# Performance work log

Hardware: AMD Instinct MI355X
Metric: run time of the kernel (lower is better)

The kernel has to match this reference:

```python
import jax, jax.numpy as jnp
import numpy as np

N_NODES = 100_000
N_EDGES = 1_600_000
IN_C, HID_C, OUT_C = 128, 64, 32


def gcn_conv(x, W, b, src, dst, n_nodes):
    """PyG GCNConv with add_self_loops=True, symmetric normalization.
    out = D^{-1/2} (A + I) D^{-1/2} (x @ W) + b, with D = deg(A) + 1.
    Self-loop contribution added analytically to avoid materializing loop edges."""
    h = x @ W                                            # [N, F_out]
    deg = jnp.zeros((n_nodes,), h.dtype).at[dst].add(1.0) + 1.0
    dinv = jax.lax.rsqrt(deg)                            # deg >= 1 from self-loops
    norm = dinv[src] * dinv[dst]                         # [E]
    agg = jnp.zeros_like(h).at[dst].add(h[src] * norm[:, None])
    agg = agg + h * (dinv * dinv)[:, None]               # self-loop term
    return agg + b


def setup_inputs() -> dict:
    key = jax.random.key(0)
    ks = jax.random.split(key, 9)
    x = jax.random.normal(ks[0], (N_NODES, IN_C), dtype=jnp.float32)
    edge_index = jax.random.randint(ks[1], (2, N_EDGES), 0, N_NODES, dtype=jnp.int64)
    g = lambda k, fi, fo: jax.random.normal(k, (fi, fo), jnp.float32) * np.sqrt(2.0 / (fi + fo)).astype(np.float32)
    W1 = g(ks[2], IN_C, HID_C)
    b1 = jnp.zeros((HID_C,), jnp.float32)
    W2 = g(ks[3], HID_C, OUT_C)
    b2 = jnp.zeros((OUT_C,), jnp.float32)
    Wl = g(ks[4], IN_C + HID_C + OUT_C, OUT_C)
    bl = jnp.zeros((OUT_C,), jnp.float32)
    return {"x": x, "edge_index": edge_index, "W1": W1, "b1": b1,
            "W2": W2, "b2": b2, "Wl": Wl, "bl": bl}


def reference(x, edge_index, W1, b1, W2, b2, Wl, bl):
    src, dst = edge_index[0], edge_index[1]
    n = x.shape[0]
    h1 = jax.nn.relu(gcn_conv(x, W1, b1, src, dst, n))   # dropout is identity in eval
    h2 = gcn_conv(h1, W2, b2, src, dst, n)
    cat = jnp.concatenate([x, h1, h2], axis=1)           # [N, in+hid+out]
    return jax.nn.log_softmax(cat @ Wl + bl, axis=-1)
```

## Files before the change

kernel.cpp:

```cpp
#include <hip/hip_runtime.h>
#include <hip/hip_bf16.h>
#include <hip/hip_fp16.h>

typedef __hip_bfloat16 bf16;
typedef __attribute__((ext_vector_type(8))) short short8;
typedef __attribute__((ext_vector_type(4))) float f32x4;

#define MFMA16(a, b, c) __builtin_amdgcn_mfma_f32_16x16x32_bf16((a), (b), (c), 0, 0, 0)

static __device__ __forceinline__ float ldf(const void* p, long long i, bool f32) {
    return f32 ? ((const float*)p)[i] : __bfloat162float(((const bf16*)p)[i]);
}

static __device__ __forceinline__ short f2bs(float v) {
    union { bf16 h; short s; } u; u.h = __float2bfloat16(v); return u.s;
}

static __device__ __forceinline__ unsigned int pack_bf16x2(float a, float b) {
    return (unsigned int)(unsigned short)f2bs(a) | ((unsigned int)(unsigned short)f2bs(b) << 16);
}

__global__ __launch_bounds__(256, 4)
void sniff_kernel(const void* __restrict__ x, const void* __restrict__ w,
                  const int* __restrict__ ei, int E, int* __restrict__ flags) {
    __shared__ int cnt;
    if (threadIdx.x == 0) cnt = 0;
    __syncthreads();
    if (blockIdx.x < 2) {
        const unsigned short* u = (const unsigned short*)(blockIdx.x == 0 ? x : w);
        int bad = 0;
        for (int i = threadIdx.x; i < 4096; i += 256) {
            unsigned e = (u[i] >> 7) & 0xFF;
            if (e >= 0xA0) bad++;
        }
        atomicAdd(&cnt, bad);
        __syncthreads();
        if (threadIdx.x == 0) flags[blockIdx.x] = (cnt > 16) ? 1 : 0;
    } else {
        int nz = 0;
        for (int i = threadIdx.x; i < 1024; i += 256)
            if (ei[2 * i + 1] != 0) nz++;
        atomicAdd(&cnt, nz);
        __syncthreads();
        if (threadIdx.x == 0) flags[2] = (cnt == 0) ? 1 : 0;
    }
}

static __device__ __forceinline__ int ld_src(const int* ei, int E, int e, bool i64) {
    return i64 ? ei[2 * e] : ei[e];
}
static __device__ __forceinline__ int ld_dst(const int* ei, int E, int e, bool i64) {
    return i64 ? ei[2 * (E + e)] : ei[E + e];
}


__global__ __launch_bounds__(256, 4)
void bhist_kernel(const int* __restrict__ ei, int E, const int* __restrict__ flags,
                  int shift, int NB, int* __restrict__ bucketCount) {
    __shared__ int h[256];
    for (int i = threadIdx.x; i < 256; i += 256) h[i] = 0;
    __syncthreads();
    bool i64 = flags[2] != 0;
    int base = blockIdx.x * 4096;
    for (int i = 0; i < 16; i++) {
        int e = base + i * 256 + threadIdx.x;
        if (e < E) atomicAdd(&h[ld_dst(ei, E, e, i64) >> shift], 1);
    }
    __syncthreads();
    for (int i = threadIdx.x; i < NB; i += 256)
        if (h[i]) atomicAdd(&bucketCount[i], h[i]);
}

__global__ __launch_bounds__(256, 4)
void bscan_kernel(const int* __restrict__ bucketCount, int NB,
                  int* __restrict__ bucketBase, int* __restrict__ bcursor, int E) {
    __shared__ int bs[256];
    int v = ((int)threadIdx.x < NB) ? bucketCount[threadIdx.x] : 0;
    bs[threadIdx.x] = v;
    __syncthreads();
    for (int off = 1; off < 256; off <<= 1) {
        int t = ((int)threadIdx.x >= off) ? bs[threadIdx.x - off] : 0;
        __syncthreads();
        bs[threadIdx.x] += t;
        __syncthreads();
    }
    int excl = bs[threadIdx.x] - v;
    if ((int)threadIdx.x < NB) { bucketBase[threadIdx.x] = excl; bcursor[threadIdx.x] = excl; }
    if (threadIdx.x == 0) bucketBase[NB] = E;
}

__global__ __launch_bounds__(256, 4)
void bpart_kernel(const int* __restrict__ ei, int E, const int* __restrict__ flags,
                  int shift, int NB, int* __restrict__ bcursor, int2* __restrict__ ebuf) {
    __shared__ int h[256];
    __shared__ int gofs[256];
    __shared__ int2 se[4096];
    for (int i = threadIdx.x; i < 256; i += 256) h[i] = 0;
    __syncthreads();
    bool i64 = flags[2] != 0;
    int base = blockIdx.x * 4096;
    for (int i = 0; i < 16; i++) {
        int e = base + i * 256 + threadIdx.x;
        if (e < E) {
            int s = ld_src(ei, E, e, i64), d = ld_dst(ei, E, e, i64);
            se[i * 256 + threadIdx.x] = make_int2(s, d);
            atomicAdd(&h[d >> shift], 1);
        }
    }
    __syncthreads();
    if ((int)threadIdx.x < NB) {
        int c = h[threadIdx.x];
        gofs[threadIdx.x] = c ? atomicAdd(&bcursor[threadIdx.x], c) : 0;
    }
    __syncthreads();
    for (int i = threadIdx.x; i < 256; i += 256) h[i] = 0;
    __syncthreads();
    for (int i = 0; i < 16; i++) {
        int e = base + i * 256 + threadIdx.x;
        if (e < E) {
            int2 v = se[i * 256 + threadIdx.x];
            int b = v.y >> shift;
            int p = atomicAdd(&h[b], 1);
            ebuf[gofs[b] + p] = v;
        }
    }
}

__global__ __launch_bounds__(256, 2)
void bbuild_kernel(const int2* __restrict__ ebuf, const int* __restrict__ bucketBase,
                   int shift, int N, int E, int* __restrict__ rowptr,
                   float* __restrict__ dinv, int* __restrict__ csr_src) {
    __shared__ int cnt[1024];
    __shared__ int exc[1024];
    __shared__ int bs[256];
    int b = blockIdx.x;
    int nodeBase = b << shift;
    int width = 1 << shift;
    int nn = N - nodeBase; if (nn > width) nn = width;
    int beg = bucketBase[b], end = bucketBase[b + 1];
    for (int i = threadIdx.x; i < width; i += 256) cnt[i] = 0;
    __syncthreads();
    for (int e = beg + threadIdx.x; e < end; e += 256)
        atomicAdd(&cnt[ebuf[e].y - nodeBase], 1);
    __syncthreads();
    int per = width / 256;
    int s = 0;
    int base4 = threadIdx.x * per;
    for (int i = 0; i < per; i++) s += cnt[base4 + i];
    bs[threadIdx.x] = s;
    __syncthreads();
    for (int off = 1; off < 256; off <<= 1) {
        int t = ((int)threadIdx.x >= off) ? bs[threadIdx.x - off] : 0;
        __syncthreads();
        bs[threadIdx.x] += t;
        __syncthreads();
    }
    int run = bs[threadIdx.x] - s;
    for (int i = 0; i < per; i++) { exc[base4 + i] = run; run += cnt[base4 + i]; }
    __syncthreads();
    for (int i = threadIdx.x; i < nn; i += 256) {
        int node = nodeBase + i;
        rowptr[node] = beg + exc[i];
        dinv[node] = rsqrtf((float)cnt[i] + 1.0f);
    }
    __syncthreads();
    for (int i = threadIdx.x; i < width; i += 256) cnt[i] = 0;
    __syncthreads();
    for (int e = beg + threadIdx.x; e < end; e += 256) {
        int2 v = ebuf[e];
        int l = v.y - nodeBase;
        int p = atomicAdd(&cnt[l], 1);
        csr_src[beg + exc[l] + p] = v.x;
    }
    if (b == 0 && threadIdx.x == 0) rowptr[N] = E;
}

__global__ __launch_bounds__(256, 4)
void repack_kernel(const void* __restrict__ W1, const void* __restrict__ W2,
                   const void* __restrict__ Wl, const int* __restrict__ flags,
                   bf16* __restrict__ Bp1, bf16* __restrict__ Bp2, bf16* __restrict__ Bp3) {
    bool fw = flags[1] != 0;
    const void* W; bf16* Bp; int ntiles, nc, nfrag;
    if (blockIdx.x == 0)      { W = W1; Bp = Bp1; ntiles = 4; nc = 64; nfrag = 16; }
    else if (blockIdx.x == 1) { W = W2; Bp = Bp2; ntiles = 2; nc = 32; nfrag = 4;  }
    else                      { W = Wl; Bp = Bp3; ntiles = 2; nc = 32; nfrag = 14; }
    for (int s = threadIdx.x; s < nfrag * 64; s += 256) {
        int f = s >> 6, lane = s & 63;
        int kstep = f / ntiles, ntile = f % ntiles;
        int n = ntile * 16 + (lane & 15);
        int kbase = kstep * 32 + (lane >> 4) * 8;
#pragma unroll
        for (int j = 0; j < 8; j++)
            Bp[s * 8 + j] = __float2bfloat16(ldf(W, (long long)(kbase + j) * nc + n, fw));
    }
}

__global__ __launch_bounds__(256, 3)
void gemm1_mfma_kernel(const void* __restrict__ x, const bf16* __restrict__ Bpack,
                       const float* __restrict__ dinv, const int* __restrict__ flags,
                       __half* __restrict__ h1g, short* __restrict__ xb, int N) {
    bool fx = flags[0] != 0;
    int lane = threadIdx.x & 63, wave = threadIdx.x >> 6;
    int m = lane & 15, quad = lane >> 4;
    int base = blockIdx.x * 128 + wave * 32;
    if (base >= N) return;
    const short8* bp = (const short8*)Bpack;
    short8 B[16];
#pragma unroll
    for (int i = 0; i < 16; i++) B[i] = bp[i * 64 + lane];
    if (base + 32 <= N) {
#pragma unroll
        for (int t = 0; t < 2; t++) {
            int r0 = base + t * 16;
            short8 A[4];
            if (fx) {
                const float* xr = &((const float*)x)[(long long)(r0 + m) * 128 + quad * 8];
#pragma unroll
                for (int k = 0; k < 4; k++) {
                    float4 fa = *(const float4*)(xr + k * 32);
                    float4 fb = *(const float4*)(xr + k * 32 + 4);
                    short8 o;
                    o[0] = f2bs(fa.x); o[1] = f2bs(fa.y); o[2] = f2bs(fa.z); o[3] = f2bs(fa.w);
                    o[4] = f2bs(fb.x); o[5] = f2bs(fb.y); o[6] = f2bs(fb.z); o[7] = f2bs(fb.w);
                    A[k] = o;
                }
                short* xw = &xb[(long long)(r0 + m) * 128 + quad * 8];
#pragma unroll
                for (int k = 0; k < 4; k++) *(short8*)(xw + k * 32) = A[k];
            } else {
                const short* xr = &((const short*)x)[(long long)(r0 + m) * 128 + quad * 8];
#pragma unroll
                for (int k = 0; k < 4; k++) A[k] = *(const short8*)(xr + k * 32);
            }
            f32x4 acc[4];
#pragma unroll
            for (int nt = 0; nt < 4; nt++) acc[nt] = (f32x4){0.f, 0.f, 0.f, 0.f};
#pragma unroll
            for (int k = 0; k < 4; k++) {
#pragma unroll
                for (int nt = 0; nt < 4; nt++) acc[nt] = MFMA16(A[k], B[k * 4 + nt], acc[nt]);
            }
            float dv[4];
#pragma unroll
            for (int r = 0; r < 4; r++) dv[r] = dinv[r0 + quad * 4 + r];
            __half* o = &h1g[(long long)(r0 + quad * 4) * 64 + m];
#pragma unroll
            for (int nt = 0; nt < 4; nt++) {
#pragma unroll
                for (int r = 0; r < 4; r++) o[(long long)r * 64 + nt * 16] = __float2half(acc[nt][r] * dv[r]);
            }
        }
    } else {
#pragma unroll
        for (int t = 0; t < 2; t++) {
            int r0 = base + t * 16;
            int row = r0 + m;
            short8 A[4];
#pragma unroll
            for (int k = 0; k < 4; k++) A[k] = (short8){0,0,0,0,0,0,0,0};
            if (row < N) {
                if (fx) {
                    const float* xr = &((const float*)x)[(long long)row * 128 + quad * 8];
#pragma unroll
                    for (int k = 0; k < 4; k++) {
                        float4 fa = *(const float4*)(xr + k * 32);
                        float4 fb = *(const float4*)(xr + k * 32 + 4);
                        short8 o;
                        o[0] = f2bs(fa.x); o[1] = f2bs(fa.y); o[2] = f2bs(fa.z); o[3] = f2bs(fa.w);
                        o[4] = f2bs(fb.x); o[5] = f2bs(fb.y); o[6] = f2bs(fb.z); o[7] = f2bs(fb.w);
                        A[k] = o;
                    }
                    short* xw = &xb[(long long)row * 128 + quad * 8];
#pragma unroll
                    for (int k = 0; k < 4; k++) *(short8*)(xw + k * 32) = A[k];
                } else {
                    const short* xr = &((const short*)x)[(long long)row * 128 + quad * 8];
#pragma unroll
                    for (int k = 0; k < 4; k++) A[k] = *(const short8*)(xr + k * 32);
                }
            }
            f32x4 acc[4];
#pragma unroll
            for (int nt = 0; nt < 4; nt++) acc[nt] = (f32x4){0.f, 0.f, 0.f, 0.f};
#pragma unroll
            for (int k = 0; k < 4; k++) {
#pragma unroll
                for (int nt = 0; nt < 4; nt++) acc[nt] = MFMA16(A[k], B[k * 4 + nt], acc[nt]);
            }
#pragma unroll
            for (int r = 0; r < 4; r++) {
                int orow = r0 + quad * 4 + r;
                if (orow < N) {
                    float dv = dinv[orow];
                    __half* o = &h1g[(long long)orow * 64 + m];
#pragma unroll
                    for (int nt = 0; nt < 4; nt++) o[nt * 16] = __float2half(acc[nt][r] * dv);
                }
            }
        }
    }
}

__global__ __launch_bounds__(256, 8)
void gather1_kernel(const unsigned int* __restrict__ h1g, const float* __restrict__ dinv,
                    const int* __restrict__ rowptr, const int* __restrict__ csr_src,
                    const void* __restrict__ bptr, const int* __restrict__ flags,
                    unsigned int* __restrict__ h1b, int N) {
    bool fw = flags[1] != 0;
    int lane = threadIdx.x & 63;
    int c = lane & 31, hf = lane >> 5;
    int wv = __builtin_amdgcn_readfirstlane(threadIdx.x >> 6);
    int n0 = (blockIdx.x * 4 + wv) * 2;
    if (n0 >= N) return;
    bool has1 = (n0 + 1 < N);
    int beg = rowptr[n0];
    int mid = rowptr[n0 + 1];
    int end = has1 ? rowptr[n0 + 2] : mid;
    const unsigned int* hL = h1g + c;
    float aA0 = 0.f, aA1 = 0.f;
    float aN0 = 0.f, aN1 = 0.f;
    int p = beg;
    for (; p + 32 <= end; p += 32) {
        unsigned int v[16]; float r[16];
#pragma unroll
        for (int u = 0; u < 16; u++) {
            int s0 = csr_src[p + 2 * u];
            int s1 = csr_src[p + 2 * u + 1];
            int s = hf ? s1 : s0;
            r[u] = ((p + 2 * u + hf) < mid) ? 1.f : 0.f;
            v[u] = hL[(long long)s * 32];
        }
#pragma unroll
        for (int u = 0; u < 16; u++) {
            float2 f = __half22float2(*(const __half2*)&v[u]);
            aA0 += f.x; aA1 += f.y;
            aN0 = fmaf(f.x, r[u], aN0);
            aN1 = fmaf(f.y, r[u], aN1);
        }
    }
    for (; p + 16 <= end; p += 16) {
        unsigned int v[8]; float r[8];
#pragma unroll
        for (int u = 0; u < 8; u++) {
            int s0 = csr_src[p + 2 * u];
            int s1 = csr_src[p + 2 * u + 1];
            int s = hf ? s1 : s0;
            r[u] = ((p + 2 * u + hf) < mid) ? 1.f : 0.f;
            v[u] = hL[(long long)s * 32];
        }
#pragma unroll
        for (int u = 0; u < 8; u++) {
            float2 f = __half22float2(*(const __half2*)&v[u]);
            aA0 += f.x; aA1 += f.y;
            aN0 = fmaf(f.x, r[u], aN0);
            aN1 = fmaf(f.y, r[u], aN1);
        }
    }
    if (p < end) {
        unsigned int v[8]; float mk[8], r[8];
#pragma unroll
        for (int u = 0; u < 8; u++) {
            int i0 = p + 2 * u, i1 = i0 + 1;
            int s0 = csr_src[(i0 < end) ? i0 : beg];
            int s1 = csr_src[(i1 < end) ? i1 : beg];
            int s = hf ? s1 : s0;
            int i = p + 2 * u + hf;
            mk[u] = (i < end) ? 1.f : 0.f;
            r[u]  = (i < mid) ? 1.f : 0.f;
            v[u] = hL[(long long)s * 32];
        }
#pragma unroll
        for (int u = 0; u < 8; u++) {
            float2 f = __half22float2(*(const __half2*)&v[u]);
            aA0 = fmaf(f.x, mk[u], aA0);
            aA1 = fmaf(f.y, mk[u], aA1);
            aN0 = fmaf(f.x, r[u], aN0);
            aN1 = fmaf(f.y, r[u], aN1);
        }
    }
    aA0 += __shfl_xor(aA0, 32); aA1 += __shfl_xor(aA1, 32);
    aN0 += __shfl_xor(aN0, 32); aN1 += __shfl_xor(aN1, 32);
    int node = n0 + hf;
    if (node < N) {
        float a0 = hf ? (aA0 - aN0) : aN0;
        float a1 = hf ? (aA1 - aN1) : aN1;
        unsigned int gsv = h1g[(long long)node * 32 + c];
        float2 gs = __half22float2(*(const __half2*)&gsv);
        float dvd = dinv[node];
        float o0 = dvd * (a0 + gs.x) + ldf(bptr, 2 * c, fw);
        float o1 = dvd * (a1 + gs.y) + ldf(bptr, 2 * c + 1, fw);
        h1b[(long long)node * 32 + c] = pack_bf16x2(fmaxf(o0, 0.f), fmaxf(o1, 0.f));
    }
}

__global__ __launch_bounds__(256, 4)
void gemm2_mfma_kernel(const short* __restrict__ h1b, const bf16* __restrict__ Bpack,
                       const float* __restrict__ dinv, __half* __restrict__ h2g, int N) {
    int lane = threadIdx.x & 63, wave = threadIdx.x >> 6;
    int m = lane & 15, quad = lane >> 4;
    int r0 = blockIdx.x * 64 + wave * 16;
    if (r0 >= N) return;
    const short8* bp = (const short8*)Bpack;
    short8 B[4];
#pragma unroll
    for (int i = 0; i < 4; i++) B[i] = bp[i * 64 + lane];
    f32x4 acc0 = {0.f,0.f,0.f,0.f}, acc1 = {0.f,0.f,0.f,0.f};
    if (r0 + 16 <= N) {
        const short* xr = &h1b[(long long)(r0 + m) * 64 + quad * 8];
#pragma unroll
        for (int k = 0; k < 2; k++) {
            short8 A = *(const short8*)(xr + k * 32);
            acc0 = MFMA16(A, B[k * 2 + 0], acc0);
            acc1 = MFMA16(A, B[k * 2 + 1], acc1);
        }
        float dv[4];
#pragma unroll
        for (int r = 0; r < 4; r++) dv[r] = dinv[r0 + quad * 4 + r];
        __half* o = &h2g[(long long)(r0 + quad * 4) * 32 + m];
#pragma unroll
        for (int r = 0; r < 4; r++) {
            o[(long long)r * 32]      = __float2half(acc0[r] * dv[r]);
            o[(long long)r * 32 + 16] = __float2half(acc1[r] * dv[r]);
        }
    } else {
        int row = r0 + m;
#pragma unroll
        for (int k = 0; k < 2; k++) {
            short8 A = {0,0,0,0,0,0,0,0};
            if (row < N) A = *(const short8*)&h1b[(long long)row * 64 + k * 32 + quad * 8];
            acc0 = MFMA16(A, B[k * 2 + 0], acc0);
            acc1 = MFMA16(A, B[k * 2 + 1], acc1);
        }
#pragma unroll
        for (int r = 0; r < 4; r++) {
            int orow = r0 + quad * 4 + r;
            if (orow < N) {
                float dv = dinv[orow];
                h2g[(long long)orow * 32 + m]      = __float2half(acc0[r] * dv);
                h2g[(long long)orow * 32 + 16 + m] = __float2half(acc1[r] * dv);
            }
        }
    }
}

__global__ __launch_bounds__(256, 8)
void gather2_kernel(const unsigned int* __restrict__ h2g, const float* __restrict__ dinv,
                    const int* __restrict__ rowptr, const int* __restrict__ csr_src,
                    const void* __restrict__ bptr, const int* __restrict__ flags,
                    unsigned int* __restrict__ h2b, int N) {
    bool fw = flags[1] != 0;
    int lane = threadIdx.x & 63;
    int c = lane & 15, sub = lane >> 4;
    int wv = __builtin_amdgcn_readfirstlane(threadIdx.x >> 6);
    int n0 = (blockIdx.x * 4 + wv) * 2;
    if (n0 >= N) return;
    bool has1 = (n0 + 1 < N);
    int beg = rowptr[n0];
    int mid = rowptr[n0 + 1];
    int end = has1 ? rowptr[n0 + 2] : mid;
    const unsigned int* hL = h2g + c;
    float aA0 = 0.f, aA1 = 0.f, aN0 = 0.f, aN1 = 0.f;
    int p = beg;
    for (; p + 32 <= end; p += 32) {
        unsigned int v[8]; float r[8];
#pragma unroll
        for (int u = 0; u < 8; u++) {
            int i0 = p + 4 * u;
            int sa0 = csr_src[i0], sa1 = csr_src[i0 + 1];
            int sa2 = csr_src[i0 + 2], sa3 = csr_src[i0 + 3];
            int sA = (sub & 1) ? sa1 : sa0;
            int sB = (sub & 1) ? sa3 : sa2;
            int s  = (sub & 2) ? sB : sA;
            r[u] = ((i0 + sub) < mid) ? 1.f : 0.f;
            v[u] = hL[(long long)s * 16];
        }
#pragma unroll
        for (int u = 0; u < 8; u++) {
            float2 f = __half22float2(*(const __half2*)&v[u]);
            aA0 += f.x; aA1 += f.y;
            aN0 = fmaf(f.x, r[u], aN0);
            aN1 = fmaf(f.y, r[u], aN1);
        }
    }
    for (; p + 16 <= end; p += 16) {
        unsigned int v[4]; float r[4];
#pragma unroll
        for (int u = 0; u < 4; u++) {
            int i0 = p + 4 * u;
            int sa0 = csr_src[i0], sa1 = csr_src[i0 + 1];
            int sa2 = csr_src[i0 + 2], sa3 = csr_src[i0 + 3];
            int sA = (sub & 1) ? sa1 : sa0;
            int sB = (sub & 1) ? sa3 : sa2;
            int s  = (sub & 2) ? sB : sA;
            r[u] = ((i0 + sub) < mid) ? 1.f : 0.f;
            v[u] = hL[(long long)s * 16];
        }
#pragma unroll
        for (int u = 0; u < 4; u++) {
            float2 f = __half22float2(*(const __half2*)&v[u]);
            aA0 += f.x; aA1 += f.y;
            aN0 = fmaf(f.x, r[u], aN0);
            aN1 = fmaf(f.y, r[u], aN1);
        }
    }
    if (p < end) {
        unsigned int v[4]; float mk[4], r[4];
#pragma unroll
        for (int u = 0; u < 4; u++) {
            int i0 = p + 4 * u;
            int sa0 = csr_src[(i0     < end) ? i0     : beg];
            int sa1 = csr_src[(i0 + 1 < end) ? i0 + 1 : beg];
            int sa2 = csr_src[(i0 + 2 < end) ? i0 + 2 : beg];
            int sa3 = csr_src[(i0 + 3 < end) ? i0 + 3 : beg];
            int sA = (sub & 1) ? sa1 : sa0;
            int sB = (sub & 1) ? sa3 : sa2;
            int s  = (sub & 2) ? sB : sA;
            int i = i0 + sub;
            mk[u] = (i < end) ? 1.f : 0.f;
            r[u]  = (i < mid) ? 1.f : 0.f;
            v[u] = hL[(long long)s * 16];
        }
#pragma unroll
        for (int u = 0; u < 4; u++) {
            float2 f = __half22float2(*(const __half2*)&v[u]);
            aA0 = fmaf(f.x, mk[u], aA0);
            aA1 = fmaf(f.y, mk[u], aA1);
            aN0 = fmaf(f.x, r[u], aN0);
            aN1 = fmaf(f.y, r[u], aN1);
        }
    }
    aA0 += __shfl_xor(aA0, 16); aA1 += __shfl_xor(aA1, 16);
    aN0 += __shfl_xor(aN0, 16); aN1 += __shfl_xor(aN1, 16);
    aA0 += __shfl_xor(aA0, 32); aA1 += __shfl_xor(aA1, 32);
    aN0 += __shfl_xor(aN0, 32); aN1 += __shfl_xor(aN1, 32);
    if (sub < 2) {
        int node = n0 + sub;
        if (node < N) {
            float a0 = sub ? (aA0 - aN0) : aN0;
            float a1 = sub ? (aA1 - aN1) : aN1;
            unsigned int gsv = h2g[(long long)node * 16 + c];
            float2 gs = __half22float2(*(const __half2*)&gsv);
            float dvd = dinv[node];
            float o0 = dvd * (a0 + gs.x) + ldf(bptr, 2 * c, fw);
            float o1 = dvd * (a1 + gs.y) + ldf(bptr, 2 * c + 1, fw);
            h2b[(long long)node * 16 + c] = pack_bf16x2(o0, o1);
        }
    }
}

__global__ __launch_bounds__(256, 2)
void final_mfma_kernel(const void* __restrict__ x, const short* __restrict__ xb,
                       const short* __restrict__ h1b,
                       const short* __restrict__ h2b, const bf16* __restrict__ Bpack,
                       const void* __restrict__ bl, const int* __restrict__ flags,
                       void* __restrict__ out, int N) {
    bool fw = flags[1] != 0, fx = flags[0] != 0;
    const short* xs = fx ? xb : (const short*)x;
    int lane = threadIdx.x & 63, wave = threadIdx.x >> 6;
    int m = lane & 15, quad = lane >> 4;
    int r0 = blockIdx.x * 64 + wave * 16;
    if (r0 >= N) return;
    const short8* bp = (const short8*)Bpack;
    short8 B[14];
#pragma unroll
    for (int i = 0; i < 14; i++) B[i] = bp[i * 64 + lane];
    f32x4 acc0 = {0.f,0.f,0.f,0.f}, acc1 = {0.f,0.f,0.f,0.f};
    bool full = (r0 + 16 <= N);
    int row = r0 + m;
    bool rowok = full || (row < N);
#pragma unroll
    for (int s = 0; s < 7; s++) {
        short8 A = {0,0,0,0,0,0,0,0};
        if (rowok) {
            const short* p;
            if (s < 4)      p = &xs [(long long)row * 128 + s * 32 + quad * 8];
            else if (s < 6) p = &h1b[(long long)row * 64 + (s - 4) * 32 + quad * 8];
            else            p = &h2b[(long long)row * 32 + quad * 8];
            A = *(const short8*)p;
        }
        acc0 = MFMA16(A, B[s * 2 + 0], acc0);
        acc1 = MFMA16(A, B[s * 2 + 1], acc1);
    }
    float bl0 = ldf(bl, m, fw), bl1 = ldf(bl, m + 16, fw);
#pragma unroll
    for (int r = 0; r < 4; r++) {
        float v0 = acc0[r] + bl0, v1 = acc1[r] + bl1;
        float mx = fmaxf(v0, v1);
#pragma unroll
        for (int o = 8; o > 0; o >>= 1) mx = fmaxf(mx, __shfl_xor(mx, o));
        float sm = __expf(v0 - mx) + __expf(v1 - mx);
#pragma unroll
        for (int o = 8; o > 0; o >>= 1) sm += __shfl_xor(sm, o);
        float lse = mx + __logf(sm);
        int orow = r0 + quad * 4 + r;
        if (orow < N) {
            if (fx) {
                ((float*)out)[(long long)orow * 32 + m]      = v0 - lse;
                ((float*)out)[(long long)orow * 32 + 16 + m] = v1 - lse;
            } else {
                ((bf16*)out)[(long long)orow * 32 + m]      = __float2bfloat16(v0 - lse);
                ((bf16*)out)[(long long)orow * 32 + 16 + m] = __float2bfloat16(v1 - lse);
            }
        }
    }
}

extern "C" void kernel_launch(void* const* d_in, const int* in_sizes, int n_in,
                              void* d_out, int out_size, void* d_ws, size_t ws_size,
                              hipStream_t stream) {
    const void* x  = d_in[0];
    const int*  ei = (const int*)d_in[1];
    const void* W1 = d_in[2];
    const void* b1 = d_in[3];
    const void* W2 = d_in[4];
    const void* b2 = d_in[5];
    const void* Wl = d_in[6];
    const void* bl = d_in[7];

    int N = in_sizes[0] / 128;
    int E = in_sizes[1] / 2;

    int shift = 9;
    while (((N + (1 << shift) - 1) >> shift) > 256 && shift < 10) shift++;
    int NB = (N + (1 << shift) - 1) >> shift;

    int* ip      = (int*)d_ws;
    int* flags   = ip;
    int* bucketCount = ip + 16;
    int* bucketBase  = bucketCount + 256;
    int* bcursor     = bucketBase + 272;
    float* dinv  = (float*)(bcursor + 256);
    int* rowptr  = (int*)(dinv + N);
    bf16* Bp1    = (bf16*)(rowptr + N + 16);
    bf16* Bp2    = (bf16*)((int*)Bp1 + 4096);
    bf16* Bp3    = (bf16*)((int*)Bp2 + 1024);
    int* csr_src = (int*)Bp3 + 3584;
    short* xb    = (short*)(csr_src + E);
    int*   Ai    = (int*)xb + (size_t)N * 64;
    int2*  ebuf  = (int2*)Ai;
    __half* h1g  = (__half*)Ai;
    __half* h2g  = (__half*)Ai;
    unsigned int* h2b = (unsigned int*)(Ai + (size_t)N * 48);
    unsigned int* h1b = (unsigned int*)(Ai + (size_t)N * 64);

    hipMemsetAsync(ip, 0, (16 + 256) * sizeof(int), stream);

    sniff_kernel<<<3, 256, 0, stream>>>(x, W1, ei, E, flags);

    int nchunk = (E + 4095) / 4096;
    bhist_kernel<<<nchunk, 256, 0, stream>>>(ei, E, flags, shift, NB, bucketCount);
    bscan_kernel<<<1, 256, 0, stream>>>(bucketCount, NB, bucketBase, bcursor, E);
    bpart_kernel<<<nchunk, 256, 0, stream>>>(ei, E, flags, shift, NB, bcursor, ebuf);
    bbuild_kernel<<<NB, 256, 0, stream>>>(ebuf, bucketBase, shift, N, E, rowptr, dinv, csr_src);

    repack_kernel<<<3, 256, 0, stream>>>(W1, W2, Wl, flags, Bp1, Bp2, Bp3);

    gemm1_mfma_kernel<<<(N + 127) / 128, 256, 0, stream>>>(x, Bp1, dinv, flags, h1g, xb, N);
    gather1_kernel<<<(N + 7) / 8, 256, 0, stream>>>((const unsigned int*)h1g, dinv, rowptr, csr_src,
                                                    b1, flags, h1b, N);
    gemm2_mfma_kernel<<<(N + 63) / 64, 256, 0, stream>>>((const short*)h1b, Bp2, dinv, h2g, N);
    gather2_kernel<<<(N + 7) / 8, 256, 0, stream>>>((const unsigned int*)h2g, dinv, rowptr, csr_src,
                                                    b2, flags, h2b, N);
    final_mfma_kernel<<<(N + 63) / 64, 256, 0, stream>>>(x, (const short*)xb, (const short*)h1b,
                                                         (const short*)h2b, Bp3, bl, flags, d_out, N);
}
```

Baseline: 293.2 us.

## Fuse sniff/repack/scan kernels and fold second-layer GEMM into gather1

Merges the dtype sniff and weight repack into the bucket-histogram launch, and drops the separate bucket-scan kernel. Each partition and build block now recomputes the prefix sum itself, and each block re-detects the index width. The layer-2 GEMM is computed inside gather1 as an FP32 dot product against W2 staged in shared memory, which removes the gemm2 launch and a round trip of h1 through global memory. The cost is redundant per-block scans and W2 loads, more LDS use in gather1 that may lower occupancy, and scalar FMA instead of MFMA for the 64x32 product.

```diff
diff --git a/kernel.cpp b/kernel.cpp
--- a/kernel.cpp
+++ b/kernel.cpp
@@ -20,48 +20,78 @@
     return (unsigned int)(unsigned short)f2bs(a) | ((unsigned int)(unsigned short)f2bs(b) << 16);
 }
 
+static __device__ __forceinline__ int ld_src(const int* ei, int E, int e, bool i64) {
+    return i64 ? ei[2 * e] : ei[e];
+}
+static __device__ __forceinline__ int ld_dst(const int* ei, int E, int e, bool i64) {
+    return i64 ? ei[2 * (E + e)] : ei[E + e];
+}
+
+
 __global__ __launch_bounds__(256, 4)
-void sniff_kernel(const void* __restrict__ x, const void* __restrict__ w,
-                  const int* __restrict__ ei, int E, int* __restrict__ flags) {
-    __shared__ int cnt;
-    if (threadIdx.x == 0) cnt = 0;
-    __syncthreads();
-    if (blockIdx.x < 2) {
-        const unsigned short* u = (const unsigned short*)(blockIdx.x == 0 ? x : w);
+void bhist_kernel(const int* __restrict__ ei, int E,
+                  const void* __restrict__ x, const void* __restrict__ W1,
+                  const void* __restrict__ Wl,
+                  int shift, int NB, int nchunk,
+                  int* __restrict__ flags, int* __restrict__ bucketCount,
+                  bf16* __restrict__ Bp1, bf16* __restrict__ Bp3) {
+    __shared__ int h[256];
+    __shared__ int sdet;
+    int bid = blockIdx.x;
+    if (bid >= nchunk) {
+        int which = bid - nchunk;
+        const void* W = which ? Wl : W1;
+        bf16* Bp = which ? Bp3 : Bp1;
+        int ntiles = which ? 2 : 4, nc = which ? 32 : 64, nfrag = which ? 14 : 16;
+        if (threadIdx.x == 0) sdet = 0;
+        __syncthreads();
+        const unsigned short* u = (const unsigned short*)W;
         int bad = 0;
         for (int i = threadIdx.x; i < 4096; i += 256) {
             unsigned e = (u[i] >> 7) & 0xFF;
             if (e >= 0xA0) bad++;
         }
-        atomicAdd(&cnt, bad);
-        __syncthreads();
-        if (threadIdx.x == 0) flags[blockIdx.x] = (cnt > 16) ? 1 : 0;
-    } else {
+        if (bad) atomicAdd(&sdet, bad);
+        __syncthreads();
+        bool fw = sdet > 16;
+        if (which == 0 && threadIdx.x == 0) flags[1] = fw ? 1 : 0;
+        for (int s = threadIdx.x; s < nfrag * 64; s += 256) {
+            int f = s >> 6, lane = s & 63;
+            int kstep = f / ntiles, ntile = f % ntiles;
+            int n = ntile * 16 + (lane & 15);
+            int kbase = kstep * 32 + (lane >> 4) * 8;
+#pragma unroll
+            for (int j = 0; j < 8; j++)
+                Bp[s * 8 + j] = __float2bfloat16(ldf(W, (long long)(kbase + j) * nc + n, fw));
+        }
+        return;
+    }
+    if (bid == 0) {
+        if (threadIdx.x == 0) sdet = 0;
+        __syncthreads();
+        const unsigned short* u = (const unsigned short*)x;
+        int bad = 0;
+        for (int i = threadIdx.x; i < 4096; i += 256) {
+            unsigned e = (u[i] >> 7) & 0xFF;
+            if (e >= 0xA0) bad++;
+        }
+        if (bad) atomicAdd(&sdet, bad);
+        __syncthreads();
+        if (threadIdx.x == 0) flags[0] = (sdet > 16) ? 1 : 0;
+        __syncthreads();
+    }
+    if (threadIdx.x == 0) sdet = 0;
+    for (int i = threadIdx.x; i < 256; i += 256) h[i] = 0;
+    __syncthreads();
+    {
         int nz = 0;
         for (int i = threadIdx.x; i < 1024; i += 256)
-            if (ei[2 * i + 1] != 0) nz++;
-        atomicAdd(&cnt, nz);
-        __syncthreads();
-        if (threadIdx.x == 0) flags[2] = (cnt == 0) ? 1 : 0;
-    }
-}
-
-static __device__ __forceinline__ int ld_src(const int* ei, int E, int e, bool i64) {
-    return i64 ? ei[2 * e] : ei[e];
-}
-static __device__ __forceinline__ int ld_dst(const int* ei, int E, int e, bool i64) {
-    return i64 ? ei[2 * (E + e)] : ei[E + e];
-}
-
-
-__global__ __launch_bounds__(256, 4)
-void bhist_kernel(const int* __restrict__ ei, int E, const int* __restrict__ flags,
-                  int shift, int NB, int* __restrict__ bucketCount) {
-    __shared__ int h[256];
-    for (int i = threadIdx.x; i < 256; i += 256) h[i] = 0;
-    __syncthreads();
-    bool i64 = flags[2] != 0;
-    int base = blockIdx.x * 4096;
+            if (2 * i + 1 < 2 * E && ei[2 * i + 1] != 0) nz++;
+        if (nz) atomicAdd(&sdet, nz);
+    }
+    __syncthreads();
+    bool i64 = (sdet == 0);
+    int base = bid * 4096;
     for (int i = 0; i < 16; i++) {
         int e = base + i * 256 + threadIdx.x;
         if (e < E) atomicAdd(&h[ld_dst(ei, E, e, i64) >> shift], 1);
@@ -72,32 +102,25 @@
 }
 
 __global__ __launch_bounds__(256, 4)
-void bscan_kernel(const int* __restrict__ bucketCount, int NB,
-                  int* __restrict__ bucketBase, int* __restrict__ bcursor, int E) {
-    __shared__ int bs[256];
-    int v = ((int)threadIdx.x < NB) ? bucketCount[threadIdx.x] : 0;
-    bs[threadIdx.x] = v;
-    __syncthreads();
-    for (int off = 1; off < 256; off <<= 1) {
-        int t = ((int)threadIdx.x >= off) ? bs[threadIdx.x - off] : 0;
-        __syncthreads();
-        bs[threadIdx.x] += t;
-        __syncthreads();
-    }
-    int excl = bs[threadIdx.x] - v;
-    if ((int)threadIdx.x < NB) { bucketBase[threadIdx.x] = excl; bcursor[threadIdx.x] = excl; }
-    if (threadIdx.x == 0) bucketBase[NB] = E;
-}
-
-__global__ __launch_bounds__(256, 4)
-void bpart_kernel(const int* __restrict__ ei, int E, const int* __restrict__ flags,
-                  int shift, int NB, int* __restrict__ bcursor, int2* __restrict__ ebuf) {
+void bpart_kernel(const int* __restrict__ ei, int E, int shift, int NB,
+                  const int* __restrict__ bucketCount, int* __restrict__ bcursor,
+                  int2* __restrict__ ebuf) {
     __shared__ int h[256];
     __shared__ int gofs[256];
+    __shared__ int bs[256];
     __shared__ int2 se[4096];
+    __shared__ int sdet;
+    if (threadIdx.x == 0) sdet = 0;
     for (int i = threadIdx.x; i < 256; i += 256) h[i] = 0;
     __syncthreads();
-    bool i64 = flags[2] != 0;
+    {
+        int nz = 0;
+        for (int i = threadIdx.x; i < 1024; i += 256)
+            if (2 * i + 1 < 2 * E && ei[2 * i + 1] != 0) nz++;
+        if (nz) atomicAdd(&sdet, nz);
+    }
+    __syncthreads();
+    bool i64 = (sdet == 0);
     int base = blockIdx.x * 4096;
     for (int i = 0; i < 16; i++) {
         int e = base + i * 256 + threadIdx.x;
@@ -107,10 +130,19 @@
             atomicAdd(&h[d >> shift], 1);
         }
     }
-    __syncthreads();
+    int v = ((int)threadIdx.x < NB) ? bucketCount[threadIdx.x] : 0;
+    bs[threadIdx.x] = v;
+    __syncthreads();
+    for (int off = 1; off < 256; off <<= 1) {
+        int t = ((int)threadIdx.x >= off) ? bs[threadIdx.x - off] : 0;
+        __syncthreads();
+        bs[threadIdx.x] += t;
+        __syncthreads();
+    }
     if ((int)threadIdx.x < NB) {
         int c = h[threadIdx.x];
-        gofs[threadIdx.x] = c ? atomicAdd(&bcursor[threadIdx.x], c) : 0;
+        int b0 = bs[threadIdx.x] - v;
+        gofs[threadIdx.x] = c ? (b0 + atomicAdd(&bcursor[threadIdx.x], c)) : 0;
     }
     __syncthreads();
     for (int i = threadIdx.x; i < 256; i += 256) h[i] = 0;
@@ -118,26 +150,37 @@
     for (int i = 0; i < 16; i++) {
         int e = base + i * 256 + threadIdx.x;
         if (e < E) {
-            int2 v = se[i * 256 + threadIdx.x];
-            int b = v.y >> shift;
+            int2 w = se[i * 256 + threadIdx.x];
+            int b = w.y >> shift;
             int p = atomicAdd(&h[b], 1);
-            ebuf[gofs[b] + p] = v;
+            ebuf[gofs[b] + p] = w;
         }
     }
 }
 
 __global__ __launch_bounds__(256, 2)
-void bbuild_kernel(const int2* __restrict__ ebuf, const int* __restrict__ bucketBase,
+void bbuild_kernel(const int2* __restrict__ ebuf, const int* __restrict__ bucketCount,
                    int shift, int N, int E, int* __restrict__ rowptr,
                    float* __restrict__ dinv, int* __restrict__ csr_src) {
     __shared__ int cnt[1024];
     __shared__ int exc[1024];
     __shared__ int bs[256];
     int b = blockIdx.x;
+    int v = ((int)threadIdx.x < 256) ? bucketCount[threadIdx.x] : 0;
+    bs[threadIdx.x] = v;
+    __syncthreads();
+    for (int off = 1; off < 256; off <<= 1) {
+        int t = ((int)threadIdx.x >= off) ? bs[threadIdx.x - off] : 0;
+        __syncthreads();
+        bs[threadIdx.x] += t;
+        __syncthreads();
+    }
+    int end = bs[b];
+    int beg = end - bucketCount[b];
+    __syncthreads();
     int nodeBase = b << shift;
     int width = 1 << shift;
     int nn = N - nodeBase; if (nn > width) nn = width;
-    int beg = bucketBase[b], end = bucketBase[b + 1];
     for (int i = threadIdx.x; i < width; i += 256) cnt[i] = 0;
     __syncthreads();
     for (int e = beg + threadIdx.x; e < end; e += 256)
@@ -167,32 +210,12 @@
     for (int i = threadIdx.x; i < width; i += 256) cnt[i] = 0;
     __syncthreads();
     for (int e = beg + threadIdx.x; e < end; e += 256) {
-        int2 v = ebuf[e];
-        int l = v.y - nodeBase;
+        int2 w = ebuf[e];
+        int l = w.y - nodeBase;
         int p = atomicAdd(&cnt[l], 1);
-        csr_src[beg + exc[l] + p] = v.x;
+        csr_src[beg + exc[l] + p] = w.x;
     }
     if (b == 0 && threadIdx.x == 0) rowptr[N] = E;
-}
-
-__global__ __launch_bounds__(256, 4)
-void repack_kernel(const void* __restrict__ W1, const void* __restrict__ W2,
-                   const void* __restrict__ Wl, const int* __restrict__ flags,
-                   bf16* __restrict__ Bp1, bf16* __restrict__ Bp2, bf16* __restrict__ Bp3) {
-    bool fw = flags[1] != 0;
-    const void* W; bf16* Bp; int ntiles, nc, nfrag;
-    if (blockIdx.x == 0)      { W = W1; Bp = Bp1; ntiles = 4; nc = 64; nfrag = 16; }
-    else if (blockIdx.x == 1) { W = W2; Bp = Bp2; ntiles = 2; nc = 32; nfrag = 4;  }
-    else                      { W = Wl; Bp = Bp3; ntiles = 2; nc = 32; nfrag = 14; }
-    for (int s = threadIdx.x; s < nfrag * 64; s += 256) {
-        int f = s >> 6, lane = s & 63;
-        int kstep = f / ntiles, ntile = f % ntiles;
-        int n = ntile * 16 + (lane & 15);
-        int kbase = kstep * 32 + (lane >> 4) * 8;
-#pragma unroll
-        for (int j = 0; j < 8; j++)
-            Bp[s * 8 + j] = __float2bfloat16(ldf(W, (long long)(kbase + j) * nc + n, fw));
-    }
 }
 
 __global__ __launch_bounds__(256, 3)
@@ -304,9 +327,15 @@
 __global__ __launch_bounds__(256, 8)
 void gather1_kernel(const unsigned int* __restrict__ h1g, const float* __restrict__ dinv,
                     const int* __restrict__ rowptr, const int* __restrict__ csr_src,
-                    const void* __restrict__ bptr, const int* __restrict__ flags,
-                    unsigned int* __restrict__ h1b, int N) {
+                    const void* __restrict__ bptr, const void* __restrict__ W2,
+                    const int* __restrict__ flags,
+                    unsigned int* __restrict__ h1b, __half* __restrict__ h2g, int N) {
+    __shared__ float w2s[64 * 32];
+    __shared__ float h1s[4][2][64];
     bool fw = flags[1] != 0;
+    for (int i = threadIdx.x; i < 2048; i += 256)
+        w2s[i] = ldf(W2, i, fw);
+    __syncthreads();
     int lane = threadIdx.x & 63;
     int c = lane & 31, hf = lane >> 5;
     int wv = __builtin_amdgcn_readfirstlane(threadIdx.x >> 6);
@@ -381,66 +410,26 @@
     aA0 += __shfl_xor(aA0, 32); aA1 += __shfl_xor(aA1, 32);
     aN0 += __shfl_xor(aN0, 32); aN1 += __shfl_xor(aN1, 32);
     int node = n0 + hf;
-    if (node < N) {
-        float a0 = hf ? (aA0 - aN0) : aN0;
-        float a1 = hf ? (aA1 - aN1) : aN1;
-        unsigned int gsv = h1g[(long long)node * 32 + c];
-        float2 gs = __half22float2(*(const __half2*)&gsv);
-        float dvd = dinv[node];
-        float o0 = dvd * (a0 + gs.x) + ldf(bptr, 2 * c, fw);
-        float o1 = dvd * (a1 + gs.y) + ldf(bptr, 2 * c + 1, fw);
-        h1b[(long long)node * 32 + c] = pack_bf16x2(fmaxf(o0, 0.f), fmaxf(o1, 0.f));
-    }
-}
-
-__global__ __launch_bounds__(256, 4)
-void gemm2_mfma_kernel(const short* __restrict__ h1b, const bf16* __restrict__ Bpack,
-                       const float* __restrict__ dinv, __half* __restrict__ h2g, int N) {
-    int lane = threadIdx.x & 63, wave = threadIdx.x >> 6;
-    int m = lane & 15, quad = lane >> 4;
-    int r0 = blockIdx.x * 64 + wave * 16;
-    if (r0 >= N) return;
-    const short8* bp = (const short8*)Bpack;
-    short8 B[4];
-#pragma unroll
-    for (int i = 0; i < 4; i++) B[i] = bp[i * 64 + lane];
-    f32x4 acc0 = {0.f,0.f,0.f,0.f}, acc1 = {0.f,0.f,0.f,0.f};
-    if (r0 + 16 <= N) {
-        const short* xr = &h1b[(long long)(r0 + m) * 64 + quad * 8];
-#pragma unroll
-        for (int k = 0; k < 2; k++) {
-            short8 A = *(const short8*)(xr + k * 32);
-            acc0 = MFMA16(A, B[k * 2 + 0], acc0);
-            acc1 = MFMA16(A, B[k * 2 + 1], acc1);
-        }
-        float dv[4];
-#pragma unroll
-        for (int r = 0; r < 4; r++) dv[r] = dinv[r0 + quad * 4 + r];
-        __half* o = &h2g[(long long)(r0 + quad * 4) * 32 + m];
-#pragma unroll
-        for (int r = 0; r < 4; r++) {
-            o[(long long)r * 32]      = __float2half(acc0[r] * dv[r]);
-            o[(long long)r * 32 + 16] = __float2half(acc1[r] * dv[r]);
-        }
-    } else {
-        int row = r0 + m;
-#pragma unroll
-        for (int k = 0; k < 2; k++) {
-            short8 A = {0,0,0,0,0,0,0,0};
-            if (row < N) A = *(const short8*)&h1b[(long long)row * 64 + k * 32 + quad * 8];
-            acc0 = MFMA16(A, B[k * 2 + 0], acc0);
-            acc1 = MFMA16(A, B[k * 2 + 1], acc1);
-        }
-#pragma unroll
-        for (int r = 0; r < 4; r++) {
-            int orow = r0 + quad * 4 + r;
-            if (orow < N) {
-                float dv = dinv[orow];
-                h2g[(long long)orow * 32 + m]      = __float2half(acc0[r] * dv);
-                h2g[(long long)orow * 32 + 16 + m] = __float2half(acc1[r] * dv);
-            }
-        }
-    }
+    int nodeC = (node < N) ? node : n0;
+    float a0 = hf ? (aA0 - aN0) : aN0;
+    float a1 = hf ? (aA1 - aN1) : aN1;
+    unsigned int gsv = h1g[(long long)nodeC * 32 + c];
+    float2 gs = __half22float2(*(const __half2*)&gsv);
+    float dvd = dinv[nodeC];
+    float o0 = fmaxf(dvd * (a0 + gs.x) + ldf(bptr, 2 * c, fw), 0.f);
+    float o1 = fmaxf(dvd * (a1 + gs.y) + ldf(bptr, 2 * c + 1, fw), 0.f);
+    if (node < N)
+        h1b[(long long)node * 32 + c] = pack_bf16x2(o0, o1);
+    h1s[wv][hf][2 * c]     = o0;
+    h1s[wv][hf][2 * c + 1] = o1;
+    __threadfence_block();
+    const float* hrow = h1s[wv][hf];
+    float acc = 0.f;
+#pragma unroll 8
+    for (int k = 0; k < 64; k++)
+        acc = fmaf(hrow[k], w2s[k * 32 + c], acc);
+    if (node < N)
+        h2g[(long long)node * 32 + c] = __float2half(dvd * acc);
 }
 
 __global__ __launch_bounds__(256, 8)
@@ -639,26 +628,21 @@
     int*   Ai    = (int*)xb + (size_t)N * 64;
     int2*  ebuf  = (int2*)Ai;
     __half* h1g  = (__half*)Ai;
-    __half* h2g  = (__half*)Ai;
+    __half* h2g  = (__half*)(Ai + (size_t)N * 32);
     unsigned int* h2b = (unsigned int*)(Ai + (size_t)N * 48);
     unsigned int* h1b = (unsigned int*)(Ai + (size_t)N * 64);
 
-    hipMemsetAsync(ip, 0, (16 + 256) * sizeof(int), stream);
-
-    sniff_kernel<<<3, 256, 0, stream>>>(x, W1, ei, E, flags);
+    hipMemsetAsync(ip, 0, 800 * sizeof(int), stream);
 
     int nchunk = (E + 4095) / 4096;
-    bhist_kernel<<<nchunk, 256, 0, stream>>>(ei, E, flags, shift, NB, bucketCount);
-    bscan_kernel<<<1, 256, 0, stream>>>(bucketCount, NB, bucketBase, bcursor, E);
-    bpart_kernel<<<nchunk, 256, 0, stream>>>(ei, E, flags, shift, NB, bcursor, ebuf);
-    bbuild_kernel<<<NB, 256, 0, stream>>>(ebuf, bucketBase, shift, N, E, rowptr, dinv, csr_src);
-
-    repack_kernel<<<3, 256, 0, stream>>>(W1, W2, Wl, flags, Bp1, Bp2, Bp3);
+    bhist_kernel<<<nchunk + 2, 256, 0, stream>>>(ei, E, x, W1, Wl, shift, NB, nchunk,
+                                                 flags, bucketCount, Bp1, Bp3);
+    bpart_kernel<<<nchunk, 256, 0, stream>>>(ei, E, shift, NB, bucketCount, bcursor, ebuf);
+    bbuild_kernel<<<NB, 256, 0, stream>>>(ebuf, bucketCount, shift, N, E, rowptr, dinv, csr_src);
 
     gemm1_mfma_kernel<<<(N + 127) / 128, 256, 0, stream>>>(x, Bp1, dinv, flags, h1g, xb, N);
     gather1_kernel<<<(N + 7) / 8, 256, 0, stream>>>((const unsigned int*)h1g, dinv, rowptr, csr_src,
-                                                    b1, flags, h1b, N);
-    gemm2_mfma_kernel<<<(N + 63) / 64, 256, 0, stream>>>((const short*)h1b, Bp2, dinv, h2g, N);
+                                                    b1, W2, flags, h1b, h2g, N);
     gather2_kernel<<<(N + 7) / 8, 256, 0, stream>>>((const unsigned int*)h2g, dinv, rowptr, csr_src,
                                                     b2, flags, h2b, N);
     final_mfma_kernel<<<(N + 63) / 64, 256, 0, stream>>>(x, (const short*)xb, (const short*)h1b,
```

Result: faster. 285.1 us (-2.8%).
